# Performance work log

Hardware: AMD Instinct MI355X
Metric: run time of the kernel (lower is better)

Reference implementation:

```python
import jax, jax.numpy as jnp
import numpy as np
from jax import lax

C = 64
EPS = 1e-6

def ln2d(x, w, b):
    # channel-wise LN over HxW per (n, c)
    mean = x.mean(axis=(2, 3), keepdims=True)
    var = ((x - mean) ** 2).mean(axis=(2, 3), keepdims=True)
    return (x - mean) / jnp.sqrt(var + EPS) * w + b

def pw(x, w, b):
    # 1x1 conv: w [O, I], b [O]
    return jnp.einsum('nihw,oi->nohw', x, w) + b[None, :, None, None]

def dwconv3(x, w, b):
    # depthwise 3x3, w [2C, 1, 3, 3]
    y = lax.conv_general_dilated(x, w, window_strides=(1, 1), padding='SAME',
                                 feature_group_count=x.shape[1],
                                 dimension_numbers=('NCHW', 'OIHW', 'NCHW'))
    return y + b[None, :, None, None]

def simple_gate(x):
    x1, x2 = jnp.split(x, 2, axis=1)
    return x1 * x2

def setup_inputs() -> dict:
    key = jax.random.key(0)
    ks = jax.random.split(key, 16)
    s = 0.05
    return {
        'x': jax.random.normal(ks[0], (8, C, 256, 256), jnp.float32),
        'ln1_w': jnp.ones((1, C, 1, 1), jnp.float32),
        'ln1_b': jnp.zeros((1, C, 1, 1), jnp.float32),
        'pw1_w': jax.random.normal(ks[1], (2 * C, C), jnp.float32) * s,
        'pw1_b': jnp.zeros((2 * C,), jnp.float32),
        'dw_w': jax.random.normal(ks[2], (2 * C, 1, 3, 3), jnp.float32) * s,
        'dw_b': jnp.zeros((2 * C,), jnp.float32),
        'sca_w': jax.random.normal(ks[3], (C, C), jnp.float32) * s,
        'sca_b': jnp.zeros((C,), jnp.float32),
        'pw2_w': jax.random.normal(ks[4], (C, C), jnp.float32) * s,
        'pw2_b': jnp.zeros((C,), jnp.float32),
        'ln2_w': jnp.ones((1, C, 1, 1), jnp.float32),
        'ln2_b': jnp.zeros((1, C, 1, 1), jnp.float32),
        'pw3_w': jax.random.normal(ks[5], (2 * C, C), jnp.float32) * s,
        'pw3_b': jnp.zeros((2 * C,), jnp.float32),
        'pw4_w': jax.random.normal(ks[6], (C, C), jnp.float32) * s,
        'pw4_b': jnp.zeros((C,), jnp.float32),
        'beta1': jax.random.normal(ks[7], (1, C, 1, 1), jnp.float32) * 0.1,
        'beta2': jax.random.normal(ks[8], (1, C, 1, 1), jnp.float32) * 0.1,
    }

def reference(x, ln1_w, ln1_b, pw1_w, pw1_b, dw_w, dw_b, sca_w, sca_b,
              pw2_w, pw2_b, ln2_w, ln2_b, pw3_w, pw3_b, pw4_w, pw4_b,
              beta1, beta2):
    y = ln2d(x, ln1_w, ln1_b)
    y = pw(y, pw1_w, pw1_b)
    y = dwconv3(y, dw_w, dw_b)
    y = simple_gate(y)
    # SCA: global avg pool -> 1x1 conv -> sigmoid scale
    s = y.mean(axis=(2, 3), keepdims=True)          # [N, C, 1, 1]
    w = jax.nn.sigmoid(pw(s, sca_w, sca_b))
    y = y * w
    y = pw(y, pw2_w, pw2_b)
    x = x + beta1 * y
    y2 = ln2d(x, ln2_w, ln2_b)
    y2 = pw(y2, pw3_w, pw3_b)
    y2 = simple_gate(y2)
    y2 = pw(y2, pw4_w, pw4_b)
    return x + beta2 * y2
```

## Files before the change

### kernel.cpp

```cpp
#include <hip/hip_runtime.h>
#include <hip/hip_bf16.h>

#define NB 8
#define CC 64
#define HWP 65536

typedef __attribute__((ext_vector_type(8))) short short8;
typedef __attribute__((ext_vector_type(4))) float f32x4;

__device__ __forceinline__ short f2bf(float f) {
  union { float f; unsigned u; } v; v.f = f;
  return (short)((v.u + 0x7FFF + ((v.u >> 16) & 1)) >> 16);
}
__device__ __forceinline__ float bf2f(unsigned short u) {
  union { unsigned u; float f; } v; v.u = ((unsigned)u) << 16; return v.f;
}

__global__ __launch_bounds__(256) void ln_stats_kernel(
    const float* __restrict__ x, const float* __restrict__ lw,
    const float* __restrict__ lb, float* __restrict__ a, float* __restrict__ b) {
  int plane = blockIdx.x;
  int c = plane & 63;
  const float4* p4 = (const float4*)(x + (size_t)plane * HWP);
  float s = 0.f, s2 = 0.f;
  for (int i = threadIdx.x; i < HWP / 4; i += 256) {
    float4 v = p4[i];
    s  += v.x + v.y + v.z + v.w;
    s2 += v.x * v.x + v.y * v.y + v.z * v.z + v.w * v.w;
  }
  for (int off = 32; off; off >>= 1) {
    s  += __shfl_down(s, off);
    s2 += __shfl_down(s2, off);
  }
  __shared__ float ls[4], ls2[4];
  int wid = threadIdx.x >> 6, lid = threadIdx.x & 63;
  if (lid == 0) { ls[wid] = s; ls2[wid] = s2; }
  __syncthreads();
  if (threadIdx.x == 0) {
    float S  = ls[0] + ls[1] + ls[2] + ls[3];
    float S2 = ls2[0] + ls2[1] + ls2[2] + ls2[3];
    float mean = S * (1.f / (float)HWP);
    float var  = S2 * (1.f / (float)HWP) - mean * mean;
    float rstd = rsqrtf(var + 1e-6f);
    float av = rstd * lw[c];
    a[plane] = av;
    b[plane] = lb[c] - mean * av;
  }
}

__global__ void fold_kernel(const float* __restrict__ w, const float* __restrict__ pb,
                            const float* __restrict__ a, const float* __restrict__ b,
                            float* __restrict__ wf, float* __restrict__ cf, int O) {
  int idx = blockIdx.x * blockDim.x + threadIdx.x;
  if (idx >= NB * O) return;
  int n = idx / O, o = idx - n * O;
  const float* an = a + n * 64;
  const float* bn = b + n * 64;
  const float* wo = w + o * 64;
  float* wfo = wf + (size_t)idx * 64;
  float cc = pb[o];
  for (int i = 0; i < 64; i++) { float wv = wo[i]; wfo[i] = wv * an[i]; cc += wv * bn[i]; }
  cf[idx] = cc;
}

__global__ __launch_bounds__(256, 2) void gemm_pw1_kernel(
    const float* __restrict__ x, const float* __restrict__ wf,
    const float* __restrict__ cf, unsigned short* __restrict__ z) {
  int n = blockIdx.y;
  int lane = threadIdx.x & 63, wid = threadIdx.x >> 6;
  int col = lane & 15, quad = lane >> 4;
  short8 a[8][2];
  const float* wfn = wf + (size_t)n * 128 * 64;
  #pragma unroll
  for (int mt = 0; mt < 8; mt++)
    #pragma unroll
    for (int ks = 0; ks < 2; ks++) {
      const float* wp = wfn + (mt * 16 + col) * 64 + ks * 32 + quad * 8;
      short8 v;
      #pragma unroll
      for (int j = 0; j < 8; j++) v[j] = f2bf(wp[j]);
      a[mt][ks] = v;
    }
  float cb[8][4];
  #pragma unroll
  for (int mt = 0; mt < 8; mt++)
    #pragma unroll
    for (int r = 0; r < 4; r++) cb[mt][r] = cf[n * 128 + mt * 16 + quad * 4 + r];
  const float* xn = x + (size_t)n * 64 * HWP;
  unsigned short* zn = z + (size_t)n * 128 * HWP;
  int pxbase = blockIdx.x * 512 + wid * 16 + col;
  for (int tile = 0; tile < 8; tile++) {
    int p = pxbase + tile * 64;
    short8 b[2];
    #pragma unroll
    for (int ks = 0; ks < 2; ks++)
      #pragma unroll
      for (int j = 0; j < 8; j++)
        b[ks][j] = f2bf(xn[(size_t)(ks * 32 + quad * 8 + j) * HWP + p]);
    f32x4 acc[8];
    #pragma unroll
    for (int mt = 0; mt < 8; mt++) {
      acc[mt] = (f32x4){0.f, 0.f, 0.f, 0.f};
      acc[mt] = __builtin_amdgcn_mfma_f32_16x16x32_bf16(a[mt][0], b[0], acc[mt], 0, 0, 0);
      acc[mt] = __builtin_amdgcn_mfma_f32_16x16x32_bf16(a[mt][1], b[1], acc[mt], 0, 0, 0);
    }
    #pragma unroll
    for (int mt = 0; mt < 8; mt++)
      #pragma unroll
      for (int r = 0; r < 4; r++)
        zn[(size_t)(mt * 16 + quad * 4 + r) * HWP + p] =
            (unsigned short)f2bf(acc[mt][r] + cb[mt][r]);
  }
}

__global__ __launch_bounds__(256) void dwgate_kernel(
    const unsigned short* __restrict__ z, const float* __restrict__ dww,
    const float* __restrict__ dwb, unsigned short* __restrict__ t,
    float* __restrict__ pooled) {
  int plane = blockIdx.x;
  int n = plane >> 6, c = plane & 63;
  int lane = threadIdx.x & 63, wv = threadIdx.x >> 6;
  const unsigned short* z0 = z + ((size_t)n * 128 + c) * HWP;
  const unsigned short* z1 = z0 + (size_t)64 * HWP;
  unsigned short* tp = t + (size_t)plane * HWP;
  float w0[9], w1[9];
  #pragma unroll
  for (int k = 0; k < 9; k++) { w0[k] = dww[c * 9 + k]; w1[k] = dww[(c + 64) * 9 + k]; }
  float bias0 = dwb[c], bias1 = dwb[c + 64];
  int r0 = wv * 64;
  int colb = lane * 4;

  float fa[3][4], la[3], ra[3];
  float fb[3][4], lb_[3], rb[3];

  auto loadrow = [&](const unsigned short* base, int h, float* f, float& l, float& r) {
    if ((unsigned)h < 256u) {
      ushort4 u = *(const ushort4*)(base + h * 256 + colb);
      f[0] = bf2f(u.x); f[1] = bf2f(u.y); f[2] = bf2f(u.z); f[3] = bf2f(u.w);
    } else {
      f[0] = f[1] = f[2] = f[3] = 0.f;
    }
    float ll = __shfl_up(f[3], 1);
    float rr = __shfl_down(f[0], 1);
    l = (lane == 0) ? 0.f : ll;
    r = (lane == 63) ? 0.f : rr;
  };

  loadrow(z0, r0 - 1, fa[0], la[0], ra[0]);
  loadrow(z1, r0 - 1, fb[0], lb_[0], rb[0]);
  loadrow(z0, r0,     fa[1], la[1], ra[1]);
  loadrow(z1, r0,     fb[1], lb_[1], rb[1]);

  float lsum = 0.f;
  #pragma unroll 2
  for (int h = r0; h < r0 + 64; h++) {
    loadrow(z0, h + 1, fa[2], la[2], ra[2]);
    loadrow(z1, h + 1, fb[2], lb_[2], rb[2]);
    float o0[4] = {bias0, bias0, bias0, bias0};
    float o1[4] = {bias1, bias1, bias1, bias1};
    #pragma unroll
    for (int rr_ = 0; rr_ < 3; rr_++) {
      float wl0 = w0[rr_ * 3], wc0 = w0[rr_ * 3 + 1], wr0 = w0[rr_ * 3 + 2];
      float wl1 = w1[rr_ * 3], wc1 = w1[rr_ * 3 + 1], wr1 = w1[rr_ * 3 + 2];
      const float* f0 = fa[rr_]; const float* f1 = fb[rr_];
      float l0 = la[rr_], r0h = ra[rr_], l1 = lb_[rr_], r1h = rb[rr_];
      o0[0] += wl0 * l0    + wc0 * f0[0] + wr0 * f0[1];
      o0[1] += wl0 * f0[0] + wc0 * f0[1] + wr0 * f0[2];
      o0[2] += wl0 * f0[1] + wc0 * f0[2] + wr0 * f0[3];
      o0[3] += wl0 * f0[2] + wc0 * f0[3] + wr0 * r0h;
      o1[0] += wl1 * l1    + wc1 * f1[0] + wr1 * f1[1];
      o1[1] += wl1 * f1[0] + wc1 * f1[1] + wr1 * f1[2];
      o1[2] += wl1 * f1[1] + wc1 * f1[2] + wr1 * f1[3];
      o1[3] += wl1 * f1[2] + wc1 * f1[3] + wr1 * r1h;
    }
    float g0 = o0[0] * o1[0], g1 = o0[1] * o1[1];
    float g2 = o0[2] * o1[2], g3 = o0[3] * o1[3];
    uint2 pk;
    pk.x = (unsigned)(unsigned short)f2bf(g0) | ((unsigned)(unsigned short)f2bf(g1) << 16);
    pk.y = (unsigned)(unsigned short)f2bf(g2) | ((unsigned)(unsigned short)f2bf(g3) << 16);
    *(uint2*)(tp + (size_t)h * 256 + colb) = pk;
    lsum += (g0 + g1) + (g2 + g3);
    #pragma unroll
    for (int i = 0; i < 4; i++) { fa[0][i] = fa[1][i]; fa[1][i] = fa[2][i];
                                  fb[0][i] = fb[1][i]; fb[1][i] = fb[2][i]; }
    la[0] = la[1]; la[1] = la[2]; ra[0] = ra[1]; ra[1] = ra[2];
    lb_[0] = lb_[1]; lb_[1] = lb_[2]; rb[0] = rb[1]; rb[1] = rb[2];
  }
  for (int off = 32; off; off >>= 1) lsum += __shfl_down(lsum, off);
  __shared__ float ls[4];
  if (lane == 0) ls[wv] = lsum;
  __syncthreads();
  if (threadIdx.x == 0) pooled[plane] = ls[0] + ls[1] + ls[2] + ls[3];
}

__global__ void sca_kernel(const float* __restrict__ pooled, const float* __restrict__ sw,
                           const float* __restrict__ sb, float* __restrict__ sca) {
  int idx = blockIdx.x * blockDim.x + threadIdx.x;
  if (idx >= 512) return;
  int n = idx >> 6, o = idx & 63;
  float s = sb[o];
  const float* pm = pooled + n * 64;
  for (int i = 0; i < 64; i++) s += sw[o * 64 + i] * pm[i] * (1.f / 65536.f);
  sca[idx] = 1.f / (1.f + expf(-s));
}

__global__ void fold_pw2_kernel(const float* __restrict__ w, const float* __restrict__ pb,
                                const float* __restrict__ sca, const float* __restrict__ beta1,
                                float* __restrict__ wf, float* __restrict__ cf) {
  int idx = blockIdx.x * blockDim.x + threadIdx.x;
  if (idx >= 512) return;
  int n = idx >> 6, o = idx & 63;
  float bt = beta1[o];
  const float* sn = sca + n * 64;
  float* wfo = wf + (size_t)idx * 64;
  for (int i = 0; i < 64; i++) wfo[i] = bt * w[o * 64 + i] * sn[i];
  cf[idx] = bt * pb[o];
}

__global__ __launch_bounds__(256, 2) void gemm_pw2_kernel(
    const unsigned short* __restrict__ t, const float* __restrict__ x,
    const float* __restrict__ wf, const float* __restrict__ cf,
    float* __restrict__ x1) {
  int n = blockIdx.y;
  int lane = threadIdx.x & 63, wid = threadIdx.x >> 6;
  int col = lane & 15, quad = lane >> 4;
  short8 a[4][2];
  const float* wfn = wf + (size_t)n * 64 * 64;
  #pragma unroll
  for (int mt = 0; mt < 4; mt++)
    #pragma unroll
    for (int ks = 0; ks < 2; ks++) {
      const float* wp = wfn + (mt * 16 + col) * 64 + ks * 32 + quad * 8;
      short8 v;
      #pragma unroll
      for (int j = 0; j < 8; j++) v[j] = f2bf(wp[j]);
      a[mt][ks] = v;
    }
  float cb[4][4];
  #pragma unroll
  for (int mt = 0; mt < 4; mt++)
    #pragma unroll
    for (int r = 0; r < 4; r++) cb[mt][r] = cf[n * 64 + mt * 16 + quad * 4 + r];
  const unsigned short* tn = t + (size_t)n * 64 * HWP;
  const float* xn = x + (size_t)n * 64 * HWP;
  float* x1n = x1 + (size_t)n * 64 * HWP;
  int pxbase = blockIdx.x * 512 + wid * 16 + col;
  for (int tile = 0; tile < 8; tile++) {
    int p = pxbase + tile * 64;
    short8 b[2];
    #pragma unroll
    for (int ks = 0; ks < 2; ks++)
      #pragma unroll
      for (int j = 0; j < 8; j++)
        b[ks][j] = (short)tn[(size_t)(ks * 32 + quad * 8 + j) * HWP + p];
    f32x4 acc[4];
    #pragma unroll
    for (int mt = 0; mt < 4; mt++) {
      acc[mt] = (f32x4){0.f, 0.f, 0.f, 0.f};
      acc[mt] = __builtin_amdgcn_mfma_f32_16x16x32_bf16(a[mt][0], b[0], acc[mt], 0, 0, 0);
      acc[mt] = __builtin_amdgcn_mfma_f32_16x16x32_bf16(a[mt][1], b[1], acc[mt], 0, 0, 0);
    }
    #pragma unroll
    for (int mt = 0; mt < 4; mt++)
      #pragma unroll
      for (int r = 0; r < 4; r++) {
        size_t idx = (size_t)(mt * 16 + quad * 4 + r) * HWP + p;
        x1n[idx] = xn[idx] + acc[mt][r] + cb[mt][r];
      }
  }
}

__global__ __launch_bounds__(256, 2) void final_mfma_kernel(
    const float* __restrict__ x1, const float* __restrict__ w3f,
    const float* __restrict__ c3f, const float* __restrict__ w4,
    const float* __restrict__ pb4, const float* __restrict__ beta2,
    float* __restrict__ out) {
  __shared__ float s_c3[128];
  __shared__ float s_b2[64];
  __shared__ float s_c4[64];
  __shared__ __align__(16) unsigned g_lds[64 * 33];
  int n = blockIdx.y;
  int lane = threadIdx.x & 63, wid = threadIdx.x >> 6;
  int col = lane & 15, quad = lane >> 4;
  if (threadIdx.x < 128) s_c3[threadIdx.x] = c3f[n * 128 + threadIdx.x];
  if (threadIdx.x < 64) { s_b2[threadIdx.x] = beta2[threadIdx.x]; s_c4[threadIdx.x] = pb4[threadIdx.x]; }
  short8 a3[8][2];
  const float* wfn = w3f + (size_t)n * 128 * 64;
  #pragma unroll
  for (int mt = 0; mt < 8; mt++)
    #pragma unroll
    for (int ks = 0; ks < 2; ks++) {
      const float* wp = wfn + (mt * 16 + col) * 64 + ks * 32 + quad * 8;
      short8 v;
      #pragma unroll
      for (int j = 0; j < 8; j++) v[j] = f2bf(wp[j]);
      a3[mt][ks] = v;
    }
  short8 a4[4][2];
  #pragma unroll
  for (int mt = 0; mt < 4; mt++)
    #pragma unroll
    for (int ks = 0; ks < 2; ks++) {
      const float* wp = w4 + (mt * 16 + col) * 64 + ks * 32 + quad * 8;
      short8 v;
      #pragma unroll
      for (int j = 0; j < 8; j++) v[j] = f2bf(wp[j]);
      a4[mt][ks] = v;
    }
  __syncthreads();
  const float* x1n = x1 + (size_t)n * 64 * HWP;
  float* outn = out + (size_t)n * 64 * HWP;
  int pxbase = blockIdx.x * 512 + wid * 16 + col;
  unsigned* grow = g_lds + (wid * 16 + col) * 33;
  for (int tile = 0; tile < 8; tile++) {
    int p = pxbase + tile * 64;
    short8 b1[2];
    #pragma unroll
    for (int ks = 0; ks < 2; ks++)
      #pragma unroll
      for (int j = 0; j < 8; j++)
        b1[ks][j] = f2bf(x1n[(size_t)(ks * 32 + quad * 8 + j) * HWP + p]);
    f32x4 acc[8];
    #pragma unroll
    for (int mt = 0; mt < 8; mt++) {
      acc[mt] = (f32x4){0.f, 0.f, 0.f, 0.f};
      acc[mt] = __builtin_amdgcn_mfma_f32_16x16x32_bf16(a3[mt][0], b1[0], acc[mt], 0, 0, 0);
      acc[mt] = __builtin_amdgcn_mfma_f32_16x16x32_bf16(a3[mt][1], b1[1], acc[mt], 0, 0, 0);
    }
    #pragma unroll
    for (int mt = 0; mt < 4; mt++)
      #pragma unroll
      for (int rr = 0; rr < 2; rr++) {
        int j0 = mt * 16 + quad * 4 + rr * 2;
        float ga = (acc[mt][rr * 2]     + s_c3[j0])     * (acc[mt + 4][rr * 2]     + s_c3[64 + j0]);
        float gb = (acc[mt][rr * 2 + 1] + s_c3[j0 + 1]) * (acc[mt + 4][rr * 2 + 1] + s_c3[64 + j0 + 1]);
        unsigned lo = (unsigned short)f2bf(ga);
        unsigned hi = (unsigned short)f2bf(gb);
        grow[j0 >> 1] = lo | (hi << 16);
      }
    __syncthreads();
    short8 b2[2];
    #pragma unroll
    for (int ks = 0; ks < 2; ks++)
      #pragma unroll
      for (int w = 0; w < 4; w++) {
        unsigned u = grow[ks * 16 + quad * 4 + w];
        b2[ks][2 * w]     = (short)(u & 0xFFFFu);
        b2[ks][2 * w + 1] = (short)(u >> 16);
      }
    __syncthreads();
    f32x4 acc2[4];
    #pragma unroll
    for (int mt = 0; mt < 4; mt++) {
      acc2[mt] = (f32x4){0.f, 0.f, 0.f, 0.f};
      acc2[mt] = __builtin_amdgcn_mfma_f32_16x16x32_bf16(a4[mt][0], b2[0], acc2[mt], 0, 0, 0);
      acc2[mt] = __builtin_amdgcn_mfma_f32_16x16x32_bf16(a4[mt][1], b2[1], acc2[mt], 0, 0, 0);
    }
    #pragma unroll
    for (int mt = 0; mt < 4; mt++)
      #pragma unroll
      for (int r = 0; r < 4; r++) {
        int o = mt * 16 + quad * 4 + r;
        size_t idx = (size_t)o * HWP + p;
        outn[idx] = x1n[idx] + s_b2[o] * (acc2[mt][r] + s_c4[o]);
      }
  }
}

extern "C" void kernel_launch(void* const* d_in, const int* in_sizes, int n_in,
                              void* d_out, int out_size, void* d_ws, size_t ws_size,
                              hipStream_t stream) {
  const float* x    = (const float*)d_in[0];
  const float* ln1w = (const float*)d_in[1];
  const float* ln1b = (const float*)d_in[2];
  const float* pw1w = (const float*)d_in[3];
  const float* pw1b = (const float*)d_in[4];
  const float* dww  = (const float*)d_in[5];
  const float* dwb  = (const float*)d_in[6];
  const float* scaw = (const float*)d_in[7];
  const float* scab = (const float*)d_in[8];
  const float* pw2w = (const float*)d_in[9];
  const float* pw2b = (const float*)d_in[10];
  const float* ln2w = (const float*)d_in[11];
  const float* ln2b = (const float*)d_in[12];
  const float* pw3w = (const float*)d_in[13];
  const float* pw3b = (const float*)d_in[14];
  const float* pw4w = (const float*)d_in[15];
  const float* pw4b = (const float*)d_in[16];
  const float* beta1= (const float*)d_in[17];
  const float* beta2= (const float*)d_in[18];
  float* out = (float*)d_out;

  char* ws = (char*)d_ws;
  unsigned short* z  = (unsigned short*)ws;
  float*          x1 = (float*)ws;
  unsigned short* t  = (unsigned short*)(ws + 134217728ull);
  float* sm = (float*)(ws + 134217728ull + 67108864ull);
  float* a1 = sm;            float* b1 = a1 + 512;
  float* w1f = b1 + 512;     float* c1f = w1f + 65536;
  float* pooled = c1f + 1024; float* sca = pooled + 512;
  float* w2f = sca + 512;    float* c2f = w2f + 32768;
  float* a2 = c2f + 512;     float* b2 = a2 + 512;
  float* w3f = b2 + 512;     float* c3f = w3f + 65536;

  hipLaunchKernelGGL(ln_stats_kernel, dim3(512), dim3(256), 0, stream, x, ln1w, ln1b, a1, b1);
  hipLaunchKernelGGL(fold_kernel, dim3(4), dim3(256), 0, stream, pw1w, pw1b, a1, b1, w1f, c1f, 128);
  hipLaunchKernelGGL(gemm_pw1_kernel, dim3(128, 8), dim3(256), 0, stream, x, w1f, c1f, z);
  hipLaunchKernelGGL(dwgate_kernel, dim3(512), dim3(256), 0, stream, z, dww, dwb, t, pooled);
  hipLaunchKernelGGL(sca_kernel, dim3(2), dim3(256), 0, stream, pooled, scaw, scab, sca);
  hipLaunchKernelGGL(fold_pw2_kernel, dim3(2), dim3(256), 0, stream, pw2w, pw2b, sca, beta1, w2f, c2f);
  hipLaunchKernelGGL(gemm_pw2_kernel, dim3(128, 8), dim3(256), 0, stream, t, x, w2f, c2f, x1);
  hipLaunchKernelGGL(ln_stats_kernel, dim3(512), dim3(256), 0, stream, x1, ln2w, ln2b, a2, b2);
  hipLaunchKernelGGL(fold_kernel, dim3(4), dim3(256), 0, stream, pw3w, pw3b, a2, b2, w3f, c3f, 128);
  hipLaunchKernelGGL(final_mfma_kernel, dim3(128, 8), dim3(256), 0, stream,
                     x1, w3f, c3f, pw4w, pw4b, beta2, out);
}
```

Measured before the change: 676.6 us.

## Emit bf16 copy of x in LN stats, pad plane strides, prefetch GEMM tiles

The first LN-stats pass now also writes a bf16 copy of x, so pw1 reads half the bytes and skips per-element conversion. All intermediate planes use a padded stride (65600) to avoid channel-strided accesses aliasing onto the same memory channels/banks. pw1 and pw2 GEMMs software-prefetch the next B tile, pw2 uses smaller blocks with higher occupancy bound, and two __syncthreads were removed from the final kernel since each thread reads only its own LDS row. Costs an extra bf16 write of x and a larger workspace footprint.

```diff
diff --git a/kernel.cpp b/kernel.cpp
--- a/kernel.cpp
+++ b/kernel.cpp
@@ -4,6 +4,7 @@
 #define NB 8
 #define CC 64
 #define HWP 65536
+#define PS 65600ull
 
 typedef __attribute__((ext_vector_type(8))) short short8;
 typedef __attribute__((ext_vector_type(4))) float f32x4;
@@ -17,16 +18,24 @@
 }
 
 __global__ __launch_bounds__(256) void ln_stats_kernel(
-    const float* __restrict__ x, const float* __restrict__ lw,
-    const float* __restrict__ lb, float* __restrict__ a, float* __restrict__ b) {
+    const float* __restrict__ x, size_t stride, const float* __restrict__ lw,
+    const float* __restrict__ lb, float* __restrict__ a, float* __restrict__ b,
+    unsigned short* __restrict__ xbf) {
   int plane = blockIdx.x;
   int c = plane & 63;
-  const float4* p4 = (const float4*)(x + (size_t)plane * HWP);
+  const float4* p4 = (const float4*)(x + (size_t)plane * stride);
+  unsigned short* xb = xbf ? (xbf + (size_t)plane * PS) : nullptr;
   float s = 0.f, s2 = 0.f;
   for (int i = threadIdx.x; i < HWP / 4; i += 256) {
     float4 v = p4[i];
     s  += v.x + v.y + v.z + v.w;
     s2 += v.x * v.x + v.y * v.y + v.z * v.z + v.w * v.w;
+    if (xb) {
+      ushort4 u;
+      u.x = (unsigned short)f2bf(v.x); u.y = (unsigned short)f2bf(v.y);
+      u.z = (unsigned short)f2bf(v.z); u.w = (unsigned short)f2bf(v.w);
+      *(ushort4*)(xb + i * 4) = u;
+    }
   }
   for (int off = 32; off; off >>= 1) {
     s  += __shfl_down(s, off);
@@ -64,7 +73,7 @@
 }
 
 __global__ __launch_bounds__(256, 2) void gemm_pw1_kernel(
-    const float* __restrict__ x, const float* __restrict__ wf,
+    const unsigned short* __restrict__ xbf, const float* __restrict__ wf,
     const float* __restrict__ cf, unsigned short* __restrict__ z) {
   int n = blockIdx.y;
   int lane = threadIdx.x & 63, wid = threadIdx.x >> 6;
@@ -86,30 +95,36 @@
   for (int mt = 0; mt < 8; mt++)
     #pragma unroll
     for (int r = 0; r < 4; r++) cb[mt][r] = cf[n * 128 + mt * 16 + quad * 4 + r];
-  const float* xn = x + (size_t)n * 64 * HWP;
-  unsigned short* zn = z + (size_t)n * 128 * HWP;
+  const unsigned short* xn = xbf + (size_t)n * 64 * PS;
+  unsigned short* zn = z + (size_t)n * 128 * PS;
   int pxbase = blockIdx.x * 512 + wid * 16 + col;
+  auto loadB = [&](int p, short8* bb) {
+    #pragma unroll
+    for (int ks = 0; ks < 2; ks++)
+      #pragma unroll
+      for (int j = 0; j < 8; j++)
+        bb[ks][j] = (short)xn[(size_t)(ks * 32 + quad * 8 + j) * PS + p];
+  };
+  short8 bcur[2], bnxt[2];
+  loadB(pxbase, bcur);
   for (int tile = 0; tile < 8; tile++) {
     int p = pxbase + tile * 64;
-    short8 b[2];
-    #pragma unroll
-    for (int ks = 0; ks < 2; ks++)
-      #pragma unroll
-      for (int j = 0; j < 8; j++)
-        b[ks][j] = f2bf(xn[(size_t)(ks * 32 + quad * 8 + j) * HWP + p]);
+    int pn = (tile < 7) ? p + 64 : pxbase;
+    loadB(pn, bnxt);
     f32x4 acc[8];
     #pragma unroll
     for (int mt = 0; mt < 8; mt++) {
       acc[mt] = (f32x4){0.f, 0.f, 0.f, 0.f};
-      acc[mt] = __builtin_amdgcn_mfma_f32_16x16x32_bf16(a[mt][0], b[0], acc[mt], 0, 0, 0);
-      acc[mt] = __builtin_amdgcn_mfma_f32_16x16x32_bf16(a[mt][1], b[1], acc[mt], 0, 0, 0);
+      acc[mt] = __builtin_amdgcn_mfma_f32_16x16x32_bf16(a[mt][0], bcur[0], acc[mt], 0, 0, 0);
+      acc[mt] = __builtin_amdgcn_mfma_f32_16x16x32_bf16(a[mt][1], bcur[1], acc[mt], 0, 0, 0);
     }
     #pragma unroll
     for (int mt = 0; mt < 8; mt++)
       #pragma unroll
       for (int r = 0; r < 4; r++)
-        zn[(size_t)(mt * 16 + quad * 4 + r) * HWP + p] =
+        zn[(size_t)(mt * 16 + quad * 4 + r) * PS + p] =
             (unsigned short)f2bf(acc[mt][r] + cb[mt][r]);
+    bcur[0] = bnxt[0]; bcur[1] = bnxt[1];
   }
 }
 
@@ -120,9 +135,9 @@
   int plane = blockIdx.x;
   int n = plane >> 6, c = plane & 63;
   int lane = threadIdx.x & 63, wv = threadIdx.x >> 6;
-  const unsigned short* z0 = z + ((size_t)n * 128 + c) * HWP;
-  const unsigned short* z1 = z0 + (size_t)64 * HWP;
-  unsigned short* tp = t + (size_t)plane * HWP;
+  const unsigned short* z0 = z + ((size_t)n * 128 + c) * PS;
+  const unsigned short* z1 = z0 + (size_t)64 * PS;
+  unsigned short* tp = t + (size_t)plane * PS;
   float w0[9], w1[9];
   #pragma unroll
   for (int k = 0; k < 9; k++) { w0[k] = dww[c * 9 + k]; w1[k] = dww[(c + 64) * 9 + k]; }
@@ -217,7 +232,7 @@
   cf[idx] = bt * pb[o];
 }
 
-__global__ __launch_bounds__(256, 2) void gemm_pw2_kernel(
+__global__ __launch_bounds__(256, 4) void gemm_pw2_kernel(
     const unsigned short* __restrict__ t, const float* __restrict__ x,
     const float* __restrict__ wf, const float* __restrict__ cf,
     float* __restrict__ x1) {
@@ -241,32 +256,38 @@
   for (int mt = 0; mt < 4; mt++)
     #pragma unroll
     for (int r = 0; r < 4; r++) cb[mt][r] = cf[n * 64 + mt * 16 + quad * 4 + r];
-  const unsigned short* tn = t + (size_t)n * 64 * HWP;
+  const unsigned short* tn = t + (size_t)n * 64 * PS;
   const float* xn = x + (size_t)n * 64 * HWP;
-  float* x1n = x1 + (size_t)n * 64 * HWP;
-  int pxbase = blockIdx.x * 512 + wid * 16 + col;
-  for (int tile = 0; tile < 8; tile++) {
+  float* x1n = x1 + (size_t)n * 64 * PS;
+  int pxbase = blockIdx.x * 256 + wid * 16 + col;
+  auto loadB = [&](int p, short8* bb) {
+    #pragma unroll
+    for (int ks = 0; ks < 2; ks++)
+      #pragma unroll
+      for (int j = 0; j < 8; j++)
+        bb[ks][j] = (short)tn[(size_t)(ks * 32 + quad * 8 + j) * PS + p];
+  };
+  short8 bcur[2], bnxt[2];
+  loadB(pxbase, bcur);
+  for (int tile = 0; tile < 4; tile++) {
     int p = pxbase + tile * 64;
-    short8 b[2];
-    #pragma unroll
-    for (int ks = 0; ks < 2; ks++)
-      #pragma unroll
-      for (int j = 0; j < 8; j++)
-        b[ks][j] = (short)tn[(size_t)(ks * 32 + quad * 8 + j) * HWP + p];
+    int pn = (tile < 3) ? p + 64 : pxbase;
+    loadB(pn, bnxt);
     f32x4 acc[4];
     #pragma unroll
     for (int mt = 0; mt < 4; mt++) {
       acc[mt] = (f32x4){0.f, 0.f, 0.f, 0.f};
-      acc[mt] = __builtin_amdgcn_mfma_f32_16x16x32_bf16(a[mt][0], b[0], acc[mt], 0, 0, 0);
-      acc[mt] = __builtin_amdgcn_mfma_f32_16x16x32_bf16(a[mt][1], b[1], acc[mt], 0, 0, 0);
+      acc[mt] = __builtin_amdgcn_mfma_f32_16x16x32_bf16(a[mt][0], bcur[0], acc[mt], 0, 0, 0);
+      acc[mt] = __builtin_amdgcn_mfma_f32_16x16x32_bf16(a[mt][1], bcur[1], acc[mt], 0, 0, 0);
     }
     #pragma unroll
     for (int mt = 0; mt < 4; mt++)
       #pragma unroll
       for (int r = 0; r < 4; r++) {
-        size_t idx = (size_t)(mt * 16 + quad * 4 + r) * HWP + p;
-        x1n[idx] = xn[idx] + acc[mt][r] + cb[mt][r];
+        int ch = mt * 16 + quad * 4 + r;
+        x1n[(size_t)ch * PS + p] = xn[(size_t)ch * HWP + p] + acc[mt][r] + cb[mt][r];
       }
+    bcur[0] = bnxt[0]; bcur[1] = bnxt[1];
   }
 }
 
@@ -308,7 +329,7 @@
       a4[mt][ks] = v;
     }
   __syncthreads();
-  const float* x1n = x1 + (size_t)n * 64 * HWP;
+  const float* x1n = x1 + (size_t)n * 64 * PS;
   float* outn = out + (size_t)n * 64 * HWP;
   int pxbase = blockIdx.x * 512 + wid * 16 + col;
   unsigned* grow = g_lds + (wid * 16 + col) * 33;
@@ -319,7 +340,7 @@
     for (int ks = 0; ks < 2; ks++)
       #pragma unroll
       for (int j = 0; j < 8; j++)
-        b1[ks][j] = f2bf(x1n[(size_t)(ks * 32 + quad * 8 + j) * HWP + p]);
+        b1[ks][j] = f2bf(x1n[(size_t)(ks * 32 + quad * 8 + j) * PS + p]);
     f32x4 acc[8];
     #pragma unroll
     for (int mt = 0; mt < 8; mt++) {
@@ -338,7 +359,6 @@
         unsigned hi = (unsigned short)f2bf(gb);
         grow[j0 >> 1] = lo | (hi << 16);
       }
-    __syncthreads();
     short8 b2[2];
     #pragma unroll
     for (int ks = 0; ks < 2; ks++)
@@ -348,7 +368,6 @@
         b2[ks][2 * w]     = (short)(u & 0xFFFFu);
         b2[ks][2 * w + 1] = (short)(u >> 16);
       }
-    __syncthreads();
     f32x4 acc2[4];
     #pragma unroll
     for (int mt = 0; mt < 4; mt++) {
@@ -361,8 +380,7 @@
       #pragma unroll
       for (int r = 0; r < 4; r++) {
         int o = mt * 16 + quad * 4 + r;
-        size_t idx = (size_t)o * HWP + p;
-        outn[idx] = x1n[idx] + s_b2[o] * (acc2[mt][r] + s_c4[o]);
+        outn[(size_t)o * HWP + p] = x1n[(size_t)o * PS + p] + s_b2[o] * (acc2[mt][r] + s_c4[o]);
       }
   }
 }
@@ -392,10 +410,11 @@
   float* out = (float*)d_out;
 
   char* ws = (char*)d_ws;
-  unsigned short* z  = (unsigned short*)ws;
-  float*          x1 = (float*)ws;
-  unsigned short* t  = (unsigned short*)(ws + 134217728ull);
-  float* sm = (float*)(ws + 134217728ull + 67108864ull);
+  unsigned short* z   = (unsigned short*)ws;
+  float*          x1  = (float*)ws;
+  unsigned short* t   = (unsigned short*)(ws + 134348800ull);
+  unsigned short* xbf = (unsigned short*)(ws + 201523200ull);
+  float* sm = (float*)(ws + 268697600ull);
   float* a1 = sm;            float* b1 = a1 + 512;
   float* w1f = b1 + 512;     float* c1f = w1f + 65536;
   float* pooled = c1f + 1024; float* sca = pooled + 512;
@@ -403,14 +422,16 @@
   float* a2 = c2f + 512;     float* b2 = a2 + 512;
   float* w3f = b2 + 512;     float* c3f = w3f + 65536;
 
-  hipLaunchKernelGGL(ln_stats_kernel, dim3(512), dim3(256), 0, stream, x, ln1w, ln1b, a1, b1);
+  hipLaunchKernelGGL(ln_stats_kernel, dim3(512), dim3(256), 0, stream,
+                     x, (size_t)HWP, ln1w, ln1b, a1, b1, xbf);
   hipLaunchKernelGGL(fold_kernel, dim3(4), dim3(256), 0, stream, pw1w, pw1b, a1, b1, w1f, c1f, 128);
-  hipLaunchKernelGGL(gemm_pw1_kernel, dim3(128, 8), dim3(256), 0, stream, x, w1f, c1f, z);
+  hipLaunchKernelGGL(gemm_pw1_kernel, dim3(128, 8), dim3(256), 0, stream, xbf, w1f, c1f, z);
   hipLaunchKernelGGL(dwgate_kernel, dim3(512), dim3(256), 0, stream, z, dww, dwb, t, pooled);
   hipLaunchKernelGGL(sca_kernel, dim3(2), dim3(256), 0, stream, pooled, scaw, scab, sca);
   hipLaunchKernelGGL(fold_pw2_kernel, dim3(2), dim3(256), 0, stream, pw2w, pw2b, sca, beta1, w2f, c2f);
-  hipLaunchKernelGGL(gemm_pw2_kernel, dim3(128, 8), dim3(256), 0, stream, t, x, w2f, c2f, x1);
-  hipLaunchKernelGGL(ln_stats_kernel, dim3(512), dim3(256), 0, stream, x1, ln2w, ln2b, a2, b2);
+  hipLaunchKernelGGL(gemm_pw2_kernel, dim3(256, 8), dim3(256), 0, stream, t, x, w2f, c2f, x1);
+  hipLaunchKernelGGL(ln_stats_kernel, dim3(512), dim3(256), 0, stream,
+                     x1, (size_t)PS, ln2w, ln2b, a2, b2, (unsigned short*)nullptr);
   hipLaunchKernelGGL(fold_kernel, dim3(4), dim3(256), 0, stream, pw3w, pw3b, a2, b2, w3f, c3f, 128);
   hipLaunchKernelGGL(final_mfma_kernel, dim3(128, 8), dim3(256), 0, stream,
                      x1, w3f, c3f, pw4w, pw4b, beta2, out);
```

Measured after the change: 685.4 us. About the same (+1.3%).
